# Optimization experiments

Measured on AMD Instinct MI355X. Metric: run time of the kernel, lower is better.

The kernel has to match this reference:

```python
import itertools
import jax, jax.numpy as jnp
import numpy as np

B, S, D = 256, 49, 448          # batch, tokens (7x7), channels
H, KD, ED = 8, 32, 128          # heads, key_dim, expanded_key_dim (attn_ratio*key_dim)
QKV_OUT = H * (KD + KD + ED)    # 1536
MLP_HID = 4 * D                 # 1792
EPS = 1e-12
SCALE = KD ** -0.5


def _bias_idxs(resolution=7):
    points = list(itertools.product(range(resolution), range(resolution)))
    offsets, idxs = {}, []
    for p1 in points:
        for p2 in points:
            off = (abs(p1[0] - p2[0]), abs(p1[1] - p2[1]))
            if off not in offsets:
                offsets[off] = len(offsets)
            idxs.append(offsets[off])
    n = len(points)
    return np.asarray(idxs, np.int32).reshape(n, n), len(offsets)


def setup_inputs() -> dict:
    key = jax.random.key(0)
    ks = jax.random.split(key, 12)
    idxs_np, n_off = _bias_idxs(7)  # [49,49], 49 offsets
    s = 0.02
    return {
        "hidden_states": jax.random.normal(ks[0], (B, S, D), jnp.float32),
        "ln2_w": jnp.ones((D,), jnp.float32),
        "ln2_b": jnp.zeros((D,), jnp.float32),
        "qkv_w": jax.random.normal(ks[1], (QKV_OUT, D), jnp.float32) * s,
        "qkv_b": jnp.zeros((QKV_OUT,), jnp.float32),
        "proj_w": jax.random.normal(ks[2], (D, H * ED), jnp.float32) * s,
        "proj_b": jnp.zeros((D,), jnp.float32),
        "attention_biases": jax.random.normal(ks[3], (H, n_off), jnp.float32) * s,
        "fc1_w": jax.random.normal(ks[4], (MLP_HID, D), jnp.float32) * s,
        "fc1_b": jnp.zeros((MLP_HID,), jnp.float32),
        "fc2_w": jax.random.normal(ks[5], (D, MLP_HID), jnp.float32) * s,
        "fc2_b": jnp.zeros((D,), jnp.float32),
        "layer_scale_1": jnp.full((D,), 1e-5, jnp.float32),
        "layer_scale_2": jnp.full((D,), 1e-5, jnp.float32),
        "attention_bias_idxs": jnp.asarray(idxs_np),  # int32 [49,49]
    }


def _layernorm(x, w, b):
    mu = jnp.mean(x, axis=-1, keepdims=True)
    var = jnp.mean(jnp.square(x - mu), axis=-1, keepdims=True)
    return (x - mu) * jax.lax.rsqrt(var + EPS) * w + b


def reference(hidden_states, ln2_w, ln2_b, qkv_w, qkv_b, proj_w, proj_b,
              attention_biases, fc1_w, fc1_b, fc2_w, fc2_b,
              layer_scale_1, layer_scale_2, attention_bias_idxs):
    # NOTE: upstream code applies norm2 before BOTH attention and MLP (faithful).
    norm = _layernorm(hidden_states, ln2_w, ln2_b)  # [B,S,D]

    qkv = (norm @ qkv_w.T + qkv_b).reshape(B, S, H, KD + KD + ED)
    q, k, v = jnp.split(qkv, [KD, 2 * KD], axis=-1)  # [B,S,H,KD/KD/ED]

    bias = attention_biases[:, attention_bias_idxs]  # [H,S,S] gathered rel-pos bias
    scores = jnp.einsum("bqhd,bkhd->bhqk", q, k) * SCALE + bias[None]
    probs = jax.nn.softmax(scores, axis=-1)          # [B,H,S,S]

    ctx = jnp.einsum("bhqk,bkhd->bqhd", probs, v).reshape(B, S, H * ED)
    attn_out = ctx @ proj_w.T + proj_b               # [B,S,D]

    out = hidden_states + layer_scale_1 * attn_out
    mlp = jax.nn.gelu(norm @ fc1_w.T + fc1_b, approximate=False) @ fc2_w.T + fc2_b
    out = out + layer_scale_2 * mlp
    return out
```

## Files before the change

### kernel.cpp

```cpp
#include <hip/hip_runtime.h>
#include <hip/hip_bf16.h>
#include <cstdint>

#define B_    256
#define S_    49
#define D_    448
#define H_    8
#define NTOK  (B_*S_)
#define QKVO  1536
#define MLPH  1792
#define SCALE_ 0.17677669529663687f

using bf16x8  = __attribute__((ext_vector_type(8))) __bf16;
using ushort8 = __attribute__((ext_vector_type(8))) unsigned short;
using f32x4   = __attribute__((ext_vector_type(4))) float;

__device__ __forceinline__ unsigned short f2bf(float f){
  uint32_t u = __builtin_bit_cast(uint32_t, f);
  u += 0x7fffu + ((u >> 16) & 1u);
  return (unsigned short)(u >> 16);
}
__device__ __forceinline__ float b2f(unsigned short b){
  uint32_t u = ((uint32_t)b) << 16;
  return __builtin_bit_cast(float, u);
}

__device__ __forceinline__ void gload_lds16(const void* g, void* l){
  __builtin_amdgcn_global_load_lds(
      (const __attribute__((address_space(1))) void*)g,
      (__attribute__((address_space(3))) void*)l, 16, 0, 0);
}

#define P_S0 688128L
#define P_S1 1490944L
#define P_S2 1949696L
#define P_S3 2752512L
#define P_S4 2932736L
#define P_S5 2936064L
#define P_S6 2936576L
#define P_S7 2969344L
__global__ __launch_bounds__(256)
void prep_k(const float* __restrict__ qkvw, const float* __restrict__ fc1w,
            const float* __restrict__ projw, const float* __restrict__ fc2w,
            const float* __restrict__ ls1, const float* __restrict__ ls2,
            const float* __restrict__ qkvb, const float* __restrict__ fc1b,
            const float* __restrict__ projb, const float* __restrict__ fc2b,
            const float* __restrict__ attb, const int* __restrict__ idxs,
            unsigned short* __restrict__ wcat, unsigned short* __restrict__ wfused,
            float* __restrict__ cbig, float* __restrict__ cbv,
            float* __restrict__ biasf){
  const long i = (long)blockIdx.x * 256 + threadIdx.x;
  if (i < P_S0){
    wcat[i] = f2bf(qkvw[i]);
  } else if (i < P_S1){
    long j = i - P_S0;
    wcat[i] = f2bf(fc1w[j]);
  } else if (i < P_S2){
    long j = i - P_S1;
    long r = j / 1024, c = j - r*1024;
    wfused[r*2816 + c] = f2bf(projw[j]*ls1[r]);
  } else if (i < P_S3){
    long j = i - P_S2;
    long r = j / 1792, c = j - r*1792;
    wfused[r*2816 + 1024 + c] = f2bf(fc2w[j]*ls2[r]);
  } else if (i < P_S4){
    long j = i - P_S3;
    wfused[448L*2816 + j] = 0;
  } else if (i < P_S5){
    long j = i - P_S4;
    cbig[j] = (j < 1536) ? qkvb[j] : fc1b[j - 1536];
  } else if (i < P_S6){
    long j = i - P_S5;
    cbv[j] = (j < 448) ? ls1[j]*projb[j] + ls2[j]*fc2b[j] : 0.f;
  } else if (i < P_S7){
    long j = i - P_S6;
    int h = (int)(j >> 12), r = (int)((j >> 6) & 63), c = (int)(j & 63);
    float v;
    if (c >= 49) v = -1e30f;
    else { int q = r < 49 ? r : 48; v = attb[h*49 + idxs[q*49 + c]]; }
    biasf[j] = v;
  }
}

__global__ __launch_bounds__(448)
void ln_k(const float* __restrict__ x, const float* __restrict__ w,
          const float* __restrict__ b, unsigned short* __restrict__ out){
  const int tok = blockIdx.x, t = threadIdx.x;
  const float v = x[(size_t)tok*448 + t];
  float s1 = v, s2 = v*v;
  #pragma unroll
  for (int o = 32; o; o >>= 1){ s1 += __shfl_xor(s1, o); s2 += __shfl_xor(s2, o); }
  __shared__ float a1[7], a2[7];
  const int wid = t >> 6;
  if ((t & 63) == 0){ a1[wid] = s1; a2[wid] = s2; }
  __syncthreads();
  float S1 = 0.f, S2 = 0.f;
  #pragma unroll
  for (int i = 0; i < 7; ++i){ S1 += a1[i]; S2 += a2[i]; }
  const float mu  = S1 * (1.f/448.f);
  const float var = S2 * (1.f/448.f) - mu*mu;
  const float rs  = rsqrtf(var + 1e-12f);
  out[(size_t)tok*448 + t] = f2bf((v - mu)*rs*w[t] + b[t]);
}

__global__ __launch_bounds__(256)
void gemm4_k(const unsigned short* __restrict__ A,
             const unsigned short* __restrict__ W,
             const float* __restrict__ bias,
             unsigned short* __restrict__ outB1,
             unsigned short* __restrict__ outB2,
             int splitBy, int nby)
{
  __shared__ char smem[65536];

  const int NB = gridDim.x;
  const int q8 = NB >> 3, r8 = NB & 7;
  const int xcd = blockIdx.x & 7, idx = blockIdx.x >> 3;
  const int wgid = (xcd < r8 ? xcd*(q8+1) : r8*(q8+1) + (xcd-r8)*q8) + idx;
  const int bx = wgid / nby, by = wgid - bx*nby;

  const int t = threadIdx.x, lane = t & 63, wid = t >> 6;
  const int wm = wid >> 1, wn = wid & 1;
  const int g = lane >> 4, li = lane & 15;
  f32x4 acc[4][4] = {};

  const int l3   = lane >> 3;
  const int sp   = (lane & 7) ^ l3;
  const int rofs = 2*l3 + (sp >> 2);
  const int cofs = (sp & 3)*8;

  auto stage = [&](int buf, int kt){
    char* Asb = smem + buf*16384;
    char* Bsb = Asb + 8192;
    const int k0 = kt*32;
    #pragma unroll
    for (int i = 0; i < 2; ++i){
      const int c = wid*2 + i;
      gload_lds16(A + (size_t)(bx*128 + c*16 + rofs)*448 + k0 + cofs, Asb + c*1024);
    }
    #pragma unroll
    for (int i = 0; i < 2; ++i){
      const int c = wid*2 + i;
      gload_lds16(W + (size_t)(by*128 + c*16 + rofs)*448 + k0 + cofs, Bsb + c*1024);
    }
  };

  const int sOff = (li >> 1)*128 + ((((li & 1)*4 + g) ^ (li >> 1)) << 4);

  stage(0, 0);
  stage(1, 1);
  int cur = 0, stg = 2;
  for (int kt = 0; kt < 14; ++kt){
    if (kt < 13) asm volatile("s_waitcnt vmcnt(4)" ::: "memory");
    else         asm volatile("s_waitcnt vmcnt(0)" ::: "memory");
    __builtin_amdgcn_s_barrier();
    if (kt + 2 < 14){ stage(stg, kt + 2); stg = (stg == 2) ? 0 : stg + 1; }
    char* Asb = smem + cur*16384;
    char* Bsb = Asb + 8192;
    bf16x8 af[4], bfr[4];
    #pragma unroll
    for (int mf = 0; mf < 4; ++mf)
      af[mf] = *reinterpret_cast<const bf16x8*>(Asb + (wm*4 + mf)*1024 + sOff);
    #pragma unroll
    for (int nf = 0; nf < 4; ++nf)
      bfr[nf] = *reinterpret_cast<const bf16x8*>(Bsb + (wn*4 + nf)*1024 + sOff);
    __builtin_amdgcn_s_setprio(1);
    #pragma unroll
    for (int mf = 0; mf < 4; ++mf)
      #pragma unroll
      for (int nf = 0; nf < 4; ++nf)
        acc[mf][nf] = __builtin_amdgcn_mfma_f32_16x16x32_bf16(af[mf], bfr[nf], acc[mf][nf], 0, 0, 0);
    __builtin_amdgcn_s_setprio(0);
    cur = (cur == 2) ? 0 : cur + 1;
  }
  __syncthreads();

  const bool dogelu = by >= splitBy;
  #pragma unroll
  for (int mf = 0; mf < 4; ++mf){
    #pragma unroll
    for (int nf = 0; nf < 4; ++nf){
      const int col = wn*64 + nf*16 + li;
      const float bi = bias[by*128 + col];
      #pragma unroll
      for (int j = 0; j < 4; ++j){
        const int row = wm*64 + mf*16 + g*4 + j;
        float v = acc[mf][nf][j] + bi;
        if (dogelu) v = 0.5f*v*(1.0f + erff(v*0.70710678118654752f));
        *reinterpret_cast<float*>(smem + row*512 + ((col*4) ^ (((row >> 2) & 3) << 6))) = v;
      }
    }
  }
  __syncthreads();
  const int lr = lane >> 4, lc = lane & 15;
  #pragma unroll
  for (int it = 0; it < 8; ++it){
    const int r = wid*32 + it*4 + lr;
    const int sw = ((r >> 2) & 3) << 6;
    const f32x4 v0 = *reinterpret_cast<const f32x4*>(smem + r*512 + ((lc*32)      ^ sw));
    const f32x4 v1 = *reinterpret_cast<const f32x4*>(smem + r*512 + ((lc*32 + 16) ^ sw));
    ushort8 u;
    #pragma unroll
    for (int k = 0; k < 4; ++k){ u[k] = f2bf(v0[k]); u[4+k] = f2bf(v1[k]); }
    const int grow = bx*128 + r;
    if (by < splitBy)
      *reinterpret_cast<ushort8*>(outB1 + (size_t)grow*QKVO + by*128 + lc*8) = u;
    else
      *reinterpret_cast<ushort8*>(outB2 + (size_t)grow*MLPH + (by - splitBy)*128 + lc*8) = u;
  }
}

__global__ __launch_bounds__(256)
void gemm1_k(const unsigned short* __restrict__ A1, int lda1, int nkt1,
             const unsigned short* __restrict__ A2, int lda2, int nkt,
             const unsigned short* __restrict__ W, int ldw,
             const float* __restrict__ bias,
             const float* __restrict__ resid, float* __restrict__ outF,
             int nby)
{
  constexpr int BN = 64, NF = 2;
  __shared__ char smem[49152];

  const int NB = gridDim.x;
  const int q8 = NB >> 3, r8 = NB & 7;
  const int xcd = blockIdx.x & 7, idx = blockIdx.x >> 3;
  const int wgid = (xcd < r8 ? xcd*(q8+1) : r8*(q8+1) + (xcd-r8)*q8) + idx;
  const int bx = wgid / nby, by = wgid - bx*nby;

  const int t = threadIdx.x, lane = t & 63, wid = t >> 6;
  const int wm = wid >> 1, wn = wid & 1;
  const int g = lane >> 4, li = lane & 15;
  f32x4 acc[4][NF] = {};

  const int srow  = lane >> 3;
  const int scolw = ((lane & 7) ^ srow) * 8;

  auto stage = [&](int buf, int kt){
    char* Asb = smem + buf*16384;
    char* Bsb = smem + 32768 + buf*(BN*128);
    const unsigned short* Ab; int lda, k0;
    if (kt < nkt1){ Ab = A1; lda = lda1; k0 = kt*64; }
    else          { Ab = A2; lda = lda2; k0 = (kt - nkt1)*64; }
    #pragma unroll
    for (int i = 0; i < 4; ++i){
      const int c = wid*4 + i;
      gload_lds16(Ab + (size_t)(bx*128 + c*8 + srow)*lda + k0 + scolw,
                  Asb + c*1024);
    }
    #pragma unroll
    for (int i = 0; i < NF; ++i){
      const int c = wid*NF + i;
      gload_lds16(W + (size_t)(by*BN + c*8 + srow)*ldw + kt*64 + scolw,
                  Bsb + c*1024);
    }
  };

  int buf = 0;
  stage(0, 0);
  for (int kt = 0; kt < nkt; ++kt){
    __syncthreads();
    if (kt + 1 < nkt) stage(buf ^ 1, kt + 1);
    char* Asb = smem + buf*16384;
    char* Bsb = smem + 32768 + buf*(BN*128);
    #pragma unroll
    for (int ks = 0; ks < 2; ++ks){
      const int kk2 = (ks*32 + g*8)*2;
      bf16x8 af[4], bfr[NF];
      #pragma unroll
      for (int mf = 0; mf < 4; ++mf){
        const int row = wm*64 + mf*16 + li;
        af[mf] = *reinterpret_cast<const bf16x8*>(
            Asb + row*128 + (kk2 ^ ((row & 7) << 4)));
      }
      #pragma unroll
      for (int nf = 0; nf < NF; ++nf){
        const int row = wn*(BN/2) + nf*16 + li;
        bfr[nf] = *reinterpret_cast<const bf16x8*>(
            Bsb + row*128 + (kk2 ^ ((row & 7) << 4)));
      }
      #pragma unroll
      for (int mf = 0; mf < 4; ++mf)
        #pragma unroll
        for (int nf = 0; nf < NF; ++nf)
          acc[mf][nf] = __builtin_amdgcn_mfma_f32_16x16x32_bf16(af[mf], bfr[nf], acc[mf][nf], 0, 0, 0);
    }
    buf ^= 1;
  }
  __syncthreads();

  const int lr = lane >> 4, lc = lane & 15;
  #pragma unroll
  for (int mf = 0; mf < 4; ++mf){
    #pragma unroll
    for (int nf = 0; nf < NF; ++nf){
      const int col = wn*32 + nf*16 + li;
      const float bi = bias[by*64 + col];
      #pragma unroll
      for (int j = 0; j < 4; ++j){
        const int rt = wm*64 + mf*16 + g*4 + j;
        *reinterpret_cast<float*>(smem + rt*256 + ((col*4) ^ (((rt >> 2) & 1) << 6)))
            = acc[mf][nf][j] + bi;
      }
    }
  }
  __syncthreads();
  #pragma unroll
  for (int i = 0; i < 8; ++i){
    const int r = wid*32 + i*4 + lr;
    const int sw = ((r >> 2) & 1) << 6;
    const f32x4 v = *reinterpret_cast<const f32x4*>(smem + r*256 + ((lc*16) ^ sw));
    const size_t o = (size_t)(bx*128 + r)*448 + by*64 + lc*4;
    const f32x4 rs = *reinterpret_cast<const f32x4*>(resid + o);
    *reinterpret_cast<f32x4*>(outF + o) = rs + v;
  }
}

__global__ __launch_bounds__(256)
void attn_mfma_k(const unsigned short* __restrict__ qkv,
                 const float* __restrict__ biasf,
                 unsigned short* __restrict__ ctx)
{
  const int bh = blockIdx.x;
  const int b = bh >> 3, h = bh & 7;
  __shared__ unsigned short QKs[64*64];
  __shared__ unsigned short Vs[64*128];
  __shared__ unsigned short Ps[64*64];
  const int t = threadIdx.x, lane = t & 63, w = t >> 6;
  const int g = lane >> 4, li = lane & 15;
  const size_t qbase = ((size_t)b*49)*QKVO + (size_t)h*192;

  for (int e = t; e < 64*8; e += 256){
    const int k = e >> 3, seg = e & 7;
    bf16x8 v = {};
    if (k < 49)
      v = *reinterpret_cast<const bf16x8*>(qkv + qbase + (size_t)k*QKVO + seg*8);
    const int byte = k*128 + ((seg ^ (k & 7)) << 4);
    *reinterpret_cast<bf16x8*>((char*)QKs + byte) = v;
  }
  for (int c = t; c < 64*16; c += 256){
    const int k = c >> 4, seg = c & 15;
    bf16x8 v = {};
    if (k < 49)
      v = *reinterpret_cast<const bf16x8*>(qkv + qbase + 64 + (size_t)k*QKVO + seg*8);
    const int byte = (k*256 + seg*16) ^ ((((unsigned)k >> 3) & 3) << 5);
    *reinterpret_cast<bf16x8*>((char*)Vs + byte) = v;
  }
  __syncthreads();

  const int qrow = w*16 + li;
  const bf16x8 afq = *reinterpret_cast<const bf16x8*>(
      (char*)QKs + qrow*128 + ((g ^ (qrow & 7)) << 4));
  f32x4 accs[4];
  #pragma unroll
  for (int nf = 0; nf < 4; ++nf){
    const int krow = nf*16 + li;
    const bf16x8 bfr = *reinterpret_cast<const bf16x8*>(
        (char*)QKs + krow*128 + (((4 + g) ^ (krow & 7)) << 4));
    f32x4 z = {};
    accs[nf] = __builtin_amdgcn_mfma_f32_16x16x32_bf16(afq, bfr, z, 0, 0, 0);
  }

  #pragma unroll
  for (int j = 0; j < 4; ++j){
    const int row = w*16 + g*4 + j;
    float sv[4];
    #pragma unroll
    for (int nf = 0; nf < 4; ++nf)
      sv[nf] = accs[nf][j]*SCALE_ + biasf[h*4096 + row*64 + nf*16 + li];
    float m = fmaxf(fmaxf(sv[0], sv[1]), fmaxf(sv[2], sv[3]));
    #pragma unroll
    for (int o = 8; o; o >>= 1) m = fmaxf(m, __shfl_xor(m, o));
    float e[4], s = 0.f;
    #pragma unroll
    for (int nf = 0; nf < 4; ++nf){ e[nf] = __expf(sv[nf] - m); s += e[nf]; }
    #pragma unroll
    for (int o = 8; o; o >>= 1) s += __shfl_xor(s, o);
    const float inv = 1.f / s;
    #pragma unroll
    for (int nf = 0; nf < 4; ++nf){
      const int byte = (row*128 + (nf*16 + li)*2) ^ ((row & 7) << 4);
      *reinterpret_cast<unsigned short*>((char*)Ps + byte) = f2bf(e[nf]*inv);
    }
  }
  __syncthreads();

  f32x4 accp[4][2] = {};
  #pragma unroll
  for (int kt = 0; kt < 2; ++kt){
    bf16x8 pa[4];
    #pragma unroll
    for (int mt = 0; mt < 4; ++mt){
      const int q = mt*16 + li;
      const int byte = (q*128 + kt*64 + g*16) ^ ((q & 7) << 4);
      pa[mt] = *reinterpret_cast<const bf16x8*>((char*)Ps + byte);
    }
    #pragma unroll
    for (int nf = 0; nf < 2; ++nf){
      const int d = w*32 + nf*16 + li;
      ushort8 vbu;
      #pragma unroll
      for (int j = 0; j < 8; ++j){
        const int k = kt*32 + g*8 + j;
        const int byte = (k*256 + d*2) ^ ((((unsigned)k >> 3) & 3) << 5);
        vbu[j] = *reinterpret_cast<const unsigned short*>((char*)Vs + byte);
      }
      const bf16x8 vb = __builtin_bit_cast(bf16x8, vbu);
      #pragma unroll
      for (int mt = 0; mt < 4; ++mt)
        accp[mt][nf] = __builtin_amdgcn_mfma_f32_16x16x32_bf16(pa[mt], vb, accp[mt][nf], 0, 0, 0);
    }
  }

  const size_t obase = ((size_t)b*49)*1024 + (size_t)h*128;
  #pragma unroll
  for (int mt = 0; mt < 4; ++mt){
    #pragma unroll
    for (int nf = 0; nf < 2; ++nf){
      #pragma unroll
      for (int j = 0; j < 4; ++j){
        const int row = mt*16 + g*4 + j;
        if (row < 49){
          const int col = w*32 + nf*16 + li;
          ctx[obase + (size_t)row*1024 + col] = f2bf(accp[mt][nf][j]);
        }
      }
    }
  }
}

extern "C" void kernel_launch(void* const* d_in, const int* in_sizes, int n_in,
                              void* d_out, int out_size, void* d_ws, size_t ws_size,
                              hipStream_t stream)
{
  const float* hidden = (const float*)d_in[0];
  const float* ln2w   = (const float*)d_in[1];
  const float* ln2b   = (const float*)d_in[2];
  const float* qkvw   = (const float*)d_in[3];
  const float* qkvb   = (const float*)d_in[4];
  const float* projw  = (const float*)d_in[5];
  const float* projb  = (const float*)d_in[6];
  const float* attb   = (const float*)d_in[7];
  const float* fc1w   = (const float*)d_in[8];
  const float* fc1b   = (const float*)d_in[9];
  const float* fc2w   = (const float*)d_in[10];
  const float* fc2b   = (const float*)d_in[11];
  const float* ls1    = (const float*)d_in[12];
  const float* ls2    = (const float*)d_in[13];
  const int*   aidx   = (const int*)d_in[14];
  float* out = (float*)d_out;

  char* p = (char*)d_ws;
  auto alloc = [&](size_t bytes){ void* r = (void*)p; p += (bytes + 255) & ~(size_t)255; return r; };
  unsigned short* wcat   = (unsigned short*)alloc((size_t)3328*448*2);
  unsigned short* wfused = (unsigned short*)alloc((size_t)512*2816*2);
  unsigned short* normb  = (unsigned short*)alloc((size_t)NTOK*448*2);
  unsigned short* qkvv   = (unsigned short*)alloc((size_t)NTOK*QKVO*2);
  unsigned short* ctx    = (unsigned short*)alloc((size_t)NTOK*1024*2);
  unsigned short* hid    = (unsigned short*)alloc((size_t)NTOK*MLPH*2);
  float*          biasf  = (float*)alloc((size_t)8*64*64*4);
  float*          cbig   = (float*)alloc((size_t)3328*4);
  float*          cbv    = (float*)alloc((size_t)512*4);

  prep_k<<<(int)(P_S7/256), 256, 0, stream>>>(qkvw, fc1w, projw, fc2w, ls1, ls2,
                                              qkvb, fc1b, projb, fc2b, attb, aidx,
                                              wcat, wfused, cbig, cbv, biasf);
  ln_k<<<NTOK, 448, 0, stream>>>(hidden, ln2w, ln2b, normb);

  gemm4_k<<<98*26, 256, 0, stream>>>(normb, wcat, cbig, qkvv, hid, 12, 26);
  attn_mfma_k<<<B_*H_, 256, 0, stream>>>(qkvv, biasf, ctx);
  gemm1_k<<<98*7, 256, 0, stream>>>(ctx, 1024, 16, hid, MLPH, 44,
                                    wfused, 2816, cbv,
                                    hidden, out, 7);
}
```

Measured before the change: 153.8 us.

## Merge weight prep with layernorm kernel and use direct-to-LDS loads in attention

The weight-conversion prep kernel and the layernorm kernel are merged into one launch, with block index selecting the role, which removes a launch and lets the two independent jobs overlap. The attention kernel now stages Q/K/V tiles with global_load_lds 16-byte direct-to-LDS loads using pre-swizzled source addresses, instead of register round-trips. Padding rows are clamped to row 48 for the load and then overwritten with zeros after a vmcnt wait. The risk is the extra zero-fill writes and correctness of the swizzle mapping.

```diff
diff --git a/kernel.cpp b/kernel.cpp
--- a/kernel.cpp
+++ b/kernel.cpp
@@ -39,68 +39,69 @@
 #define P_S5 2936064L
 #define P_S6 2936576L
 #define P_S7 2969344L
-__global__ __launch_bounds__(256)
-void prep_k(const float* __restrict__ qkvw, const float* __restrict__ fc1w,
-            const float* __restrict__ projw, const float* __restrict__ fc2w,
-            const float* __restrict__ ls1, const float* __restrict__ ls2,
-            const float* __restrict__ qkvb, const float* __restrict__ fc1b,
-            const float* __restrict__ projb, const float* __restrict__ fc2b,
-            const float* __restrict__ attb, const int* __restrict__ idxs,
-            unsigned short* __restrict__ wcat, unsigned short* __restrict__ wfused,
-            float* __restrict__ cbig, float* __restrict__ cbv,
-            float* __restrict__ biasf){
-  const long i = (long)blockIdx.x * 256 + threadIdx.x;
-  if (i < P_S0){
-    wcat[i] = f2bf(qkvw[i]);
-  } else if (i < P_S1){
-    long j = i - P_S0;
-    wcat[i] = f2bf(fc1w[j]);
-  } else if (i < P_S2){
-    long j = i - P_S1;
-    long r = j / 1024, c = j - r*1024;
-    wfused[r*2816 + c] = f2bf(projw[j]*ls1[r]);
-  } else if (i < P_S3){
-    long j = i - P_S2;
-    long r = j / 1792, c = j - r*1792;
-    wfused[r*2816 + 1024 + c] = f2bf(fc2w[j]*ls2[r]);
-  } else if (i < P_S4){
-    long j = i - P_S3;
-    wfused[448L*2816 + j] = 0;
-  } else if (i < P_S5){
-    long j = i - P_S4;
-    cbig[j] = (j < 1536) ? qkvb[j] : fc1b[j - 1536];
-  } else if (i < P_S6){
-    long j = i - P_S5;
-    cbv[j] = (j < 448) ? ls1[j]*projb[j] + ls2[j]*fc2b[j] : 0.f;
-  } else if (i < P_S7){
-    long j = i - P_S6;
-    int h = (int)(j >> 12), r = (int)((j >> 6) & 63), c = (int)(j & 63);
-    float v;
-    if (c >= 49) v = -1e30f;
-    else { int q = r < 49 ? r : 48; v = attb[h*49 + idxs[q*49 + c]]; }
-    biasf[j] = v;
-  }
-}
-
+#define PREP_BLKS 6628
 __global__ __launch_bounds__(448)
-void ln_k(const float* __restrict__ x, const float* __restrict__ w,
-          const float* __restrict__ b, unsigned short* __restrict__ out){
-  const int tok = blockIdx.x, t = threadIdx.x;
-  const float v = x[(size_t)tok*448 + t];
-  float s1 = v, s2 = v*v;
-  #pragma unroll
-  for (int o = 32; o; o >>= 1){ s1 += __shfl_xor(s1, o); s2 += __shfl_xor(s2, o); }
-  __shared__ float a1[7], a2[7];
-  const int wid = t >> 6;
-  if ((t & 63) == 0){ a1[wid] = s1; a2[wid] = s2; }
-  __syncthreads();
-  float S1 = 0.f, S2 = 0.f;
-  #pragma unroll
-  for (int i = 0; i < 7; ++i){ S1 += a1[i]; S2 += a2[i]; }
-  const float mu  = S1 * (1.f/448.f);
-  const float var = S2 * (1.f/448.f) - mu*mu;
-  const float rs  = rsqrtf(var + 1e-12f);
-  out[(size_t)tok*448 + t] = f2bf((v - mu)*rs*w[t] + b[t]);
+void prepln_k(const float* __restrict__ x, const float* __restrict__ lw,
+              const float* __restrict__ lb, unsigned short* __restrict__ normb,
+              const float* __restrict__ qkvw, const float* __restrict__ fc1w,
+              const float* __restrict__ projw, const float* __restrict__ fc2w,
+              const float* __restrict__ ls1, const float* __restrict__ ls2,
+              const float* __restrict__ qkvb, const float* __restrict__ fc1b,
+              const float* __restrict__ projb, const float* __restrict__ fc2b,
+              const float* __restrict__ attb, const int* __restrict__ idxs,
+              unsigned short* __restrict__ wcat, unsigned short* __restrict__ wfused,
+              float* __restrict__ cbig, float* __restrict__ cbv,
+              float* __restrict__ biasf){
+  const int bid = blockIdx.x, t = threadIdx.x;
+  if (bid < NTOK){
+    const float v = x[(size_t)bid*448 + t];
+    float s1 = v, s2 = v*v;
+    #pragma unroll
+    for (int o = 32; o; o >>= 1){ s1 += __shfl_xor(s1, o); s2 += __shfl_xor(s2, o); }
+    __shared__ float a1[7], a2[7];
+    const int wid = t >> 6;
+    if ((t & 63) == 0){ a1[wid] = s1; a2[wid] = s2; }
+    __syncthreads();
+    float S1 = 0.f, S2 = 0.f;
+    #pragma unroll
+    for (int i = 0; i < 7; ++i){ S1 += a1[i]; S2 += a2[i]; }
+    const float mu  = S1 * (1.f/448.f);
+    const float var = S2 * (1.f/448.f) - mu*mu;
+    const float rs  = rsqrtf(var + 1e-12f);
+    normb[(size_t)bid*448 + t] = f2bf((v - mu)*rs*lw[t] + lb[t]);
+  } else {
+    const long i = (long)(bid - NTOK)*448 + t;
+    if (i < P_S0){
+      wcat[i] = f2bf(qkvw[i]);
+    } else if (i < P_S1){
+      long j = i - P_S0;
+      wcat[i] = f2bf(fc1w[j]);
+    } else if (i < P_S2){
+      long j = i - P_S1;
+      long r = j / 1024;
+      wfused[r*2816 + (j - r*1024)] = f2bf(projw[j]*ls1[r]);
+    } else if (i < P_S3){
+      long j = i - P_S2;
+      long r = j / 1792;
+      wfused[r*2816 + 1024 + (j - r*1792)] = f2bf(fc2w[j]*ls2[r]);
+    } else if (i < P_S4){
+      long j = i - P_S3;
+      wfused[448L*2816 + j] = 0;
+    } else if (i < P_S5){
+      long j = i - P_S4;
+      cbig[j] = (j < 1536) ? qkvb[j] : fc1b[j - 1536];
+    } else if (i < P_S6){
+      long j = i - P_S5;
+      cbv[j] = (j < 448) ? ls1[j]*projb[j] + ls2[j]*fc2b[j] : 0.f;
+    } else if (i < P_S7){
+      long j = i - P_S6;
+      int h = (int)(j >> 12), r = (int)((j >> 6) & 63), c = (int)(j & 63);
+      float v;
+      if (c >= 49) v = -1e30f;
+      else { int q = r < 49 ? r : 48; v = attb[h*49 + idxs[q*49 + c]]; }
+      biasf[j] = v;
+    }
+  }
 }
 
 __global__ __launch_bounds__(256)
@@ -329,21 +330,35 @@
   const int g = lane >> 4, li = lane & 15;
   const size_t qbase = ((size_t)b*49)*QKVO + (size_t)h*192;
 
-  for (int e = t; e < 64*8; e += 256){
-    const int k = e >> 3, seg = e & 7;
-    bf16x8 v = {};
-    if (k < 49)
-      v = *reinterpret_cast<const bf16x8*>(qkv + qbase + (size_t)k*QKVO + seg*8);
-    const int byte = k*128 + ((seg ^ (k & 7)) << 4);
-    *reinterpret_cast<bf16x8*>((char*)QKs + byte) = v;
-  }
-  for (int c = t; c < 64*16; c += 256){
-    const int k = c >> 4, seg = c & 15;
-    bf16x8 v = {};
-    if (k < 49)
-      v = *reinterpret_cast<const bf16x8*>(qkv + qbase + 64 + (size_t)k*QKVO + seg*8);
-    const int byte = (k*256 + seg*16) ^ ((((unsigned)k >> 3) & 3) << 5);
-    *reinterpret_cast<bf16x8*>((char*)Vs + byte) = v;
+  {
+    const int kk = lane >> 3, ss = lane & 7;
+    #pragma unroll
+    for (int i = 0; i < 2; ++i){
+      const int kb = (w*2 + i)*8;
+      const int k  = kb + kk;
+      const int ks = k < 49 ? k : 48;
+      gload_lds16(qkv + qbase + (size_t)ks*QKVO + ((ss ^ (k & 7))*8),
+                  (char*)QKs + kb*128);
+    }
+    const int kv = lane >> 4, sv = lane & 15;
+    #pragma unroll
+    for (int i = 0; i < 4; ++i){
+      const int kb = (w*4 + i)*4;
+      const int k  = kb + kv;
+      const int ks = k < 49 ? k : 48;
+      const int swz = (((unsigned)k >> 3) & 3) << 1;
+      gload_lds16(qkv + qbase + 64 + (size_t)ks*QKVO + ((sv ^ swz)*8),
+                  (char*)Vs + kb*256);
+    }
+  }
+  asm volatile("s_waitcnt vmcnt(0)" ::: "memory");
+  for (int e = t; e < 15*8; e += 256){
+    const int k = 49 + (e >> 3), s = e & 7;
+    *reinterpret_cast<bf16x8*>((char*)QKs + k*128 + s*16) = (bf16x8){};
+  }
+  for (int e = t; e < 15*16; e += 256){
+    const int k = 49 + (e >> 4), s = e & 15;
+    *reinterpret_cast<bf16x8*>((char*)Vs + k*256 + s*16) = (bf16x8){};
   }
   __syncthreads();
 
@@ -461,10 +476,10 @@
   float*          cbig   = (float*)alloc((size_t)3328*4);
   float*          cbv    = (float*)alloc((size_t)512*4);
 
-  prep_k<<<(int)(P_S7/256), 256, 0, stream>>>(qkvw, fc1w, projw, fc2w, ls1, ls2,
-                                              qkvb, fc1b, projb, fc2b, attb, aidx,
-                                              wcat, wfused, cbig, cbv, biasf);
-  ln_k<<<NTOK, 448, 0, stream>>>(hidden, ln2w, ln2b, normb);
+  prepln_k<<<NTOK + PREP_BLKS, 448, 0, stream>>>(hidden, ln2w, ln2b, normb,
+                                                 qkvw, fc1w, projw, fc2w, ls1, ls2,
+                                                 qkvb, fc1b, projb, fc2b, attb, aidx,
+                                                 wcat, wfused, cbig, cbv, biasf);
 
   gemm4_k<<<98*26, 256, 0, stream>>>(normb, wcat, cbig, qkvv, hid, 12, 26);
   attn_mfma_k<<<B_*H_, 256, 0, stream>>>(qkvv, biasf, ctx);
```

Measured after the change: 150.6 us, median of 2. -2.1%, faster.
